# Performance work log

Hardware: AMD Instinct MI355X
Metric: run time of the kernel (lower is better)

Reference implementation:

```python
import jax, jax.numpy as jnp
import numpy as np

B, T, C, H = 128, 256, 384, 6
HS = C // H  # 64
EPS = 1e-5


def _ln(x, g, b):
    mu = jnp.mean(x, axis=-1, keepdims=True)
    var = jnp.mean(jnp.square(x - mu), axis=-1, keepdims=True)
    return (x - mu) * jax.lax.rsqrt(var + EPS) * g + b


def setup_inputs() -> dict:
    key = jax.random.key(0)
    ks = jax.random.split(key, 12)
    s = 0.02
    return {
        "x": jax.random.normal(ks[0], (B, T, C), jnp.float32),
        "wq": jax.random.normal(ks[1], (H, C, HS), jnp.float32) * s,
        "wk": jax.random.normal(ks[2], (H, C, HS), jnp.float32) * s,
        "wv": jax.random.normal(ks[3], (H, C, HS), jnp.float32) * s,
        "w_proj": jax.random.normal(ks[4], (C, C), jnp.float32) * s,
        "b_proj": jax.random.normal(ks[5], (C,), jnp.float32) * s,
        "w1": jax.random.normal(ks[6], (C, 4 * C), jnp.float32) * s,
        "b1": jax.random.normal(ks[7], (4 * C,), jnp.float32) * s,
        "w2": jax.random.normal(ks[8], (4 * C, C), jnp.float32) * s,
        "b2": jax.random.normal(ks[9], (C,), jnp.float32) * s,
        "ln1_g": 1.0 + jax.random.normal(ks[10], (C,), jnp.float32) * s,
        "ln1_b": jnp.zeros((C,), jnp.float32),
        "ln2_g": 1.0 + jax.random.normal(ks[11], (C,), jnp.float32) * s,
        "ln2_b": jnp.zeros((C,), jnp.float32),
    }


def reference(x, wq, wk, wv, w_proj, b_proj, w1, b1, w2, b2, ln1_g, ln1_b, ln2_g, ln2_b):
    # --- attention sublayer (dropout = identity, eval mode) ---
    h = _ln(x, ln1_g, ln1_b)                              # (B,T,C)
    q = jnp.einsum("btc,hcd->bhtd", h, wq)               # (B,H,T,HS)
    k = jnp.einsum("btc,hcd->bhtd", h, wk)
    v = jnp.einsum("btc,hcd->bhtd", h, wv)
    # NOTE: original scales by n_embed**-0.5 (C), not head_size**-0.5
    wei = jnp.einsum("bhtd,bhsd->bhts", q, k) * (C ** -0.5)  # (B,H,T,T)
    tril = jnp.tril(jnp.ones((T, T), bool))
    wei = jnp.where(tril, wei, -jnp.inf)
    # NOTE: original applies softmax over torch dim=1 of (B,T,T) = query axis
    wei = jax.nn.softmax(wei, axis=2)
    attn = jnp.einsum("bhts,bhsd->bhtd", wei, v)          # (B,H,T,HS)
    attn = attn.transpose(0, 2, 1, 3).reshape(B, T, C)    # head-concat order
    x = x + attn @ w_proj + b_proj
    # --- MLP sublayer ---
    h2 = _ln(x, ln2_g, ln2_b)
    x = x + jax.nn.relu(h2 @ w1 + b1) @ w2 + b2
    return x
```

## Files before the change

### kernel.cpp

```cpp
#include <hip/hip_runtime.h>

#define BB 128
#define TT 256
#define CCH 384
#define NHH 6
#define HSZ 64
#define BTT (BB*TT)
#define QKVLD 1152

typedef unsigned short u16;
typedef unsigned int   u32;
typedef __attribute__((ext_vector_type(8))) short  short8;
typedef __attribute__((ext_vector_type(4))) float  floatx4;

__device__ __forceinline__ u16 f2bf(float f) {
  union { float f; u32 i; } v; v.f = f; u32 x = v.i;
  return (u16)((x + 0x7fffu + ((x >> 16) & 1u)) >> 16);
}
__device__ __forceinline__ float bf2f(u16 w) {
  union { u32 i; float f; } v; v.i = ((u32)w) << 16; return v.f;
}

__device__ __forceinline__ void gll16(const u16* g, u16* l) {
  __builtin_amdgcn_global_load_lds((const __attribute__((address_space(1))) void*)g,
                                   (__attribute__((address_space(3))) void*)l, 16, 0, 0);
}

template <int INBF>
__global__ __launch_bounds__(256) void ln_kernel(const void* __restrict__ xv,
                                                 const float* __restrict__ g,
                                                 const float* __restrict__ b,
                                                 u16* __restrict__ out) {
  int row = blockIdx.x * 4 + (threadIdx.x >> 6);
  int lane = threadIdx.x & 63;
  float vals[6];
  float sum = 0.f;
  if (INBF) {
    const u16* xr = (const u16*)xv + (size_t)row * CCH;
#pragma unroll
    for (int i = 0; i < 6; ++i) { vals[i] = bf2f(xr[lane + (i << 6)]); sum += vals[i]; }
  } else {
    const float* xr = (const float*)xv + (size_t)row * CCH;
#pragma unroll
    for (int i = 0; i < 6; ++i) { vals[i] = xr[lane + (i << 6)]; sum += vals[i]; }
  }
#pragma unroll
  for (int off = 32; off; off >>= 1) sum += __shfl_xor(sum, off);
  float mean = sum * (1.f / 384.f);
  float vs = 0.f;
#pragma unroll
  for (int i = 0; i < 6; ++i) { float d = vals[i] - mean; vs += d * d; }
#pragma unroll
  for (int off = 32; off; off >>= 1) vs += __shfl_xor(vs, off);
  float rinv = rsqrtf(vs * (1.f / 384.f) + 1e-5f);
  u16* orow = out + (size_t)row * CCH;
#pragma unroll
  for (int i = 0; i < 6; ++i) {
    int c = lane + (i << 6);
    orow[c] = f2bf((vals[i] - mean) * rinv * g[c] + b[c]);
  }
}

__global__ void repack_all(const float* __restrict__ wq, const float* __restrict__ wk,
                           const float* __restrict__ wv, const float* __restrict__ wproj,
                           const float* __restrict__ w1, const float* __restrict__ w2,
                           u16* __restrict__ wqkv_t, u16* __restrict__ wp_t,
                           u16* __restrict__ w1_t, u16* __restrict__ w2_t) {
  int idx = blockIdx.x * 256 + threadIdx.x;
  if (idx < 147456) {
    int n = idx / CCH, kk = idx % CCH;
    size_t src = ((size_t)(n >> 6) * CCH + kk) * 64 + (n & 63);
    wqkv_t[idx]          = f2bf(wq[src]);
    wqkv_t[idx + 147456] = f2bf(wk[src]);
    wqkv_t[idx + 294912] = f2bf(wv[src]);
  } else if (idx < 294912) {
    int i = idx - 147456;
    int n = i / CCH, kk = i % CCH;
    wp_t[i] = f2bf(wproj[(size_t)kk * CCH + n]);
  } else if (idx < 294912 + 589824) {
    int i = idx - 294912;
    int n = i / CCH, kk = i % CCH;
    w1_t[i] = f2bf(w1[(size_t)kk * 1536 + n]);
  } else if (idx < 294912 + 2 * 589824) {
    int i = idx - 294912 - 589824;
    int n = i / 1536, kk = i % 1536;
    w2_t[i] = f2bf(w2[(size_t)kk * CCH + n]);
  }
}

template <int BIAS, int RES, int RELU, int OUTBF, int RESBF>
__global__ __launch_bounds__(256, 4) void gemm_mfma(const u16* __restrict__ A,
                                                    const u16* __restrict__ W,
                                                    const float* __restrict__ bias,
                                                    const void* __restrict__ resv,
                                                    void* __restrict__ outv,
                                                    int M, int N, int K) {
  __shared__ __align__(16) u16 As[2][128 * 32];
  __shared__ __align__(16) u16 Bs[2][128 * 32];
  const int tid = threadIdx.x;
  const int lane = tid & 63;
  const int w = tid >> 6;
  const int wr = w >> 1, wc = w & 1;

  const int gx = gridDim.x;
  const int nwg = gx * gridDim.y;
  const int bid = blockIdx.y * gx + blockIdx.x;
  const int lin = (bid & 7) * (nwg >> 3) + (bid >> 3);
  const int m0 = (lin / gx) * 128, n0 = (lin % gx) * 128;

  const int lm = lane & 15, qd = lane >> 4;

  floatx4 acc[4][4];
  floatx4 zero4 = {0.f, 0.f, 0.f, 0.f};
#pragma unroll
  for (int i = 0; i < 4; ++i)
#pragma unroll
    for (int j = 0; j < 4; ++j) acc[i][j] = zero4;

  const u16* srcA[2];
  const u16* srcB[2];
#pragma unroll
  for (int c = 0; c < 2; ++c) {
    int row = 32 * w + 16 * c + (lane >> 2);
    int ch = (lane & 3) ^ ((row >> 1) & 3);
    srcA[c] = A + (size_t)(m0 + row) * K + ch * 8;
    srcB[c] = W + (size_t)(n0 + row) * K + ch * 8;
  }
  const int dAB = (32 * w) * 32;

#pragma unroll
  for (int c = 0; c < 2; ++c) gll16(srcA[c], &As[0][dAB + 512 * c]);
#pragma unroll
  for (int c = 0; c < 2; ++c) gll16(srcB[c], &Bs[0][dAB + 512 * c]);

  int ib = 0;
  for (int k0 = 0; k0 < K; k0 += 32, ib ^= 1) {
    __syncthreads();
    int kn = k0 + 32;
    if (kn < K) {
      int nb = ib ^ 1;
#pragma unroll
      for (int c = 0; c < 2; ++c) gll16(srcA[c] + kn, &As[nb][dAB + 512 * c]);
#pragma unroll
      for (int c = 0; c < 2; ++c) gll16(srcB[c] + kn, &Bs[nb][dAB + 512 * c]);
    }
    short8 af[4], bf[4];
#pragma unroll
    for (int i = 0; i < 4; ++i) {
      int rm = 64 * wr + 16 * i + lm;
      af[i] = *(const short8*)&As[ib][rm * 32 + (qd ^ ((rm >> 1) & 3)) * 8];
    }
#pragma unroll
    for (int j = 0; j < 4; ++j) {
      int rn = 64 * wc + 16 * j + lm;
      bf[j] = *(const short8*)&Bs[ib][rn * 32 + (qd ^ ((rn >> 1) & 3)) * 8];
    }
#pragma unroll
    for (int i = 0; i < 4; ++i)
#pragma unroll
      for (int j = 0; j < 4; ++j)
        acc[i][j] = __builtin_amdgcn_mfma_f32_16x16x32_bf16(af[i], bf[j], acc[i][j], 0, 0, 0);
  }

#pragma unroll
  for (int i = 0; i < 4; ++i) {
    int row0 = m0 + 64 * wr + 16 * i + qd * 4;
#pragma unroll
    for (int j = 0; j < 4; ++j) {
      int col = n0 + 64 * wc + 16 * j + lm;
      float bb = 0.f;
      if (BIAS) bb = bias[col];
#pragma unroll
      for (int r = 0; r < 4; ++r) {
        size_t idx = (size_t)(row0 + r) * N + col;
        float val = acc[i][j][r] + bb;
        if (RES) val += RESBF ? bf2f(((const u16*)resv)[idx]) : ((const float*)resv)[idx];
        if (RELU) val = fmaxf(val, 0.f);
        if (OUTBF) ((u16*)outv)[idx] = f2bf(val);
        else       ((float*)outv)[idx] = val;
      }
    }
  }
}

__global__ __launch_bounds__(512, 1) void fused_mlp(const u16* __restrict__ h,
                                                    const u16* __restrict__ w1t,
                                                    const float* __restrict__ b1,
                                                    const u16* __restrict__ w2t,
                                                    const float* __restrict__ b2,
                                                    const u16* __restrict__ x2,
                                                    float* __restrict__ out) {
  __shared__ __align__(16) u16 Ah[128 * 384];
  __shared__ __align__(16) u16 Us[128 * 128];
  const int tid = threadIdx.x;
  const int lane = tid & 63;
  const int w = tid >> 6;
  const int lm = lane & 15, qd = lane >> 4;
  const int m0 = blockIdx.x * 128;

#pragma unroll
  for (int rnd = 0; rnd < 12; ++rnd) {
    int wbase = rnd * 4096 + w * 512;
    int off = wbase + lane * 8;
    int row = off / 384;
    int slot = (off - row * 384) >> 3;
    const u16* src = h + (size_t)(m0 + row) * 384 + ((slot ^ (row & 7)) << 3);
    gll16(src, &Ah[wbase]);
  }
  asm volatile("s_waitcnt vmcnt(0)" ::: "memory");
  __syncthreads();

  floatx4 zero4 = {0.f, 0.f, 0.f, 0.f};
  floatx4 ao[8][3];
#pragma unroll
  for (int i = 0; i < 8; ++i)
#pragma unroll
    for (int j = 0; j < 3; ++j) ao[i][j] = zero4;

  const int wr1 = w >> 2, wc1 = w & 3;

  for (int c = 0; c < 12; ++c) {
    floatx4 au[4][2];
#pragma unroll
    for (int i = 0; i < 4; ++i) { au[i][0] = zero4; au[i][1] = zero4; }
    const u16* w1p = w1t + (size_t)(c * 128 + 32 * wc1 + lm) * 384 + qd * 8;
#pragma unroll
    for (int ks = 0; ks < 12; ++ks) {
      short8 bf0 = *(const short8*)(w1p + ks * 32);
      short8 bf1 = *(const short8*)(w1p + 16 * 384 + ks * 32);
      int sl = ((ks * 4 + qd) ^ (lm & 7)) << 3;
#pragma unroll
      for (int i = 0; i < 4; ++i) {
        short8 af = *(const short8*)&Ah[(64 * wr1 + 16 * i + lm) * 384 + sl];
        au[i][0] = __builtin_amdgcn_mfma_f32_16x16x32_bf16(af, bf0, au[i][0], 0, 0, 0);
        au[i][1] = __builtin_amdgcn_mfma_f32_16x16x32_bf16(af, bf1, au[i][1], 0, 0, 0);
      }
    }
    float bv0 = b1[c * 128 + 32 * wc1 + lm];
    float bv1 = b1[c * 128 + 32 * wc1 + 16 + lm];
#pragma unroll
    for (int i = 0; i < 4; ++i)
#pragma unroll
      for (int j = 0; j < 2; ++j) {
        int ucol = 32 * wc1 + 16 * j + lm;
        float bv = j ? bv1 : bv0;
#pragma unroll
        for (int r = 0; r < 4; ++r) {
          int urow = 64 * wr1 + 16 * i + qd * 4 + r;
          float v = fmaxf(au[i][j][r] + bv, 0.f);
          Us[urow * 128 + ((((ucol >> 3) ^ (urow & 7)) << 3) | (ucol & 7))] = f2bf(v);
        }
      }
    __syncthreads();

    const u16* w2p = w2t + (size_t)(48 * w + lm) * 1536 + c * 128 + qd * 8;
#pragma unroll
    for (int ks = 0; ks < 4; ++ks) {
      short8 bb0 = *(const short8*)(w2p + ks * 32);
      short8 bb1 = *(const short8*)(w2p + (size_t)16 * 1536 + ks * 32);
      short8 bb2 = *(const short8*)(w2p + (size_t)32 * 1536 + ks * 32);
      int sl = ((ks * 4 + qd) ^ (lm & 7)) << 3;
#pragma unroll
      for (int i = 0; i < 8; ++i) {
        short8 uf = *(const short8*)&Us[(16 * i + lm) * 128 + sl];
        ao[i][0] = __builtin_amdgcn_mfma_f32_16x16x32_bf16(uf, bb0, ao[i][0], 0, 0, 0);
        ao[i][1] = __builtin_amdgcn_mfma_f32_16x16x32_bf16(uf, bb1, ao[i][1], 0, 0, 0);
        ao[i][2] = __builtin_amdgcn_mfma_f32_16x16x32_bf16(uf, bb2, ao[i][2], 0, 0, 0);
      }
    }
    __syncthreads();
  }

#pragma unroll
  for (int i = 0; i < 8; ++i)
#pragma unroll
    for (int jj = 0; jj < 3; ++jj) {
      int col = 48 * w + 16 * jj + lm;
      float bb = b2[col];
#pragma unroll
      for (int r = 0; r < 4; ++r) {
        size_t idx = (size_t)(m0 + 16 * i + qd * 4 + r) * 384 + col;
        out[idx] = ao[i][jj][r] + bb + bf2f(x2[idx]);
      }
    }
}

#define ASCALE 0.051031036307982884f

__global__ __launch_bounds__(1024) void attn_mfma(const u16* __restrict__ qkv,
                                                  u16* __restrict__ out) {
  __shared__ __align__(16) char lds_raw[36864 + 20480 + 2048];
  u16*   Ks       = (u16*)lds_raw;
  u16*   VT       = (u16*)lds_raw;
  float* partials = (float*)(lds_raw + 36864);
  u16*   stage    = (u16*)(lds_raw + 36864);
  float* gmax     = (float*)(lds_raw + 57344);
  float* linv     = (float*)(lds_raw + 58368);

  const int tid = threadIdx.x;
  const int lane = tid & 63;
  const int w = tid >> 6;
  const int lm = lane & 15, qd = lane >> 4;
  const int b = blockIdx.x / NHH, h = blockIdx.x % NHH;
  const size_t rowbase = (size_t)b * TT;
  const u16* qp = qkv + rowbase * QKVLD + h * HSZ;
  const u16* kp = qp + 384;
  const u16* vp = qp + 768;

  {
    int s = tid >> 2, c4 = tid & 3;
    const u16* src = kp + (size_t)s * QKVLD;
    *(uint4*)&Ks[s * 72 + c4 * 8]       = *(const uint4*)(src + c4 * 8);
    *(uint4*)&Ks[s * 72 + (c4 + 4) * 8] = *(const uint4*)(src + (c4 + 4) * 8);
  }
  short8 qf0, qf1;
  {
    const u16* qrow = qp + (size_t)(16 * w + lm) * QKVLD + qd * 8;
    qf0 = *(const short8*)(qrow);
    qf1 = *(const short8*)(qrow + 32);
  }
  __syncthreads();

  floatx4 acc[16];
  floatx4 zero4 = {0.f, 0.f, 0.f, 0.f};
#pragma unroll
  for (int tc = 0; tc < 16; ++tc) acc[tc] = zero4;

#pragma unroll
  for (int tc = 0; tc < 16; ++tc) {
    if (tc <= w) {
      int sr = 16 * tc + lm;
      short8 kf0 = *(const short8*)&Ks[sr * 72 + qd * 8];
      short8 kf1 = *(const short8*)&Ks[sr * 72 + 32 + qd * 8];
      acc[tc] = __builtin_amdgcn_mfma_f32_16x16x32_bf16(qf0, kf0, acc[tc], 0, 0, 0);
      acc[tc] = __builtin_amdgcn_mfma_f32_16x16x32_bf16(qf1, kf1, acc[tc], 0, 0, 0);
    }
  }

  const int rb = 16 * w + qd * 4;
  float pmax[16];
#pragma unroll
  for (int tc = 0; tc < 16; ++tc) {
    float m = -1e30f;
    if (tc <= w) {
      int sc = 16 * tc + lm;
#pragma unroll
      for (int r = 0; r < 4; ++r) {
        float vv = acc[tc][r] * ASCALE;
        vv = (rb + r >= sc) ? vv : -1e30f;
        acc[tc][r] = vv;
        m = fmaxf(m, vv);
      }
    }
    m = fmaxf(m, __shfl_xor(m, 16));
    m = fmaxf(m, __shfl_xor(m, 32));
    pmax[tc] = m;
  }
  if (lane < 16) {
#pragma unroll
    for (int tc = 0; tc < 16; ++tc) partials[w * 256 + tc * 16 + lane] = pmax[tc];
  }
  __syncthreads();
  if (tid < 256) {
    float m = partials[tid];
#pragma unroll
    for (int i = 1; i < 16; ++i) m = fmaxf(m, partials[i * 256 + tid]);
    gmax[tid] = m;
  }
  __syncthreads();

  float psum[16];
#pragma unroll
  for (int tc = 0; tc < 16; ++tc) {
    float s = 0.f;
    if (tc <= w) {
      float gm = gmax[tc * 16 + lm];
#pragma unroll
      for (int r = 0; r < 4; ++r) {
        float e = (acc[tc][r] > -1e29f) ? __expf(acc[tc][r] - gm) : 0.f;
        acc[tc][r] = e;
        s += e;
      }
    }
    s += __shfl_xor(s, 16);
    s += __shfl_xor(s, 32);
    psum[tc] = s;
  }
  if (lane < 16) {
#pragma unroll
    for (int tc = 0; tc < 16; ++tc) partials[w * 256 + tc * 16 + lane] = psum[tc];
  }
  __syncthreads();
  if (tid < 256) {
    float s = partials[tid];
#pragma unroll
    for (int i = 1; i < 16; ++i) s += partials[i * 256 + tid];
    linv[tid] = 1.f / s;
  }
  __syncthreads();

  {
    int s = tid >> 2, dg = (tid & 3) * 16;
    const u16* vrow = vp + (size_t)s * QKVLD + dg;
    u16 tmp[16];
    *(uint4*)&tmp[0] = *(const uint4*)(vrow);
    *(uint4*)&tmp[8] = *(const uint4*)(vrow + 8);
#pragma unroll
    for (int j = 0; j < 16; ++j) VT[(dg + j) * 264 + s] = tmp[j];
  }
  __syncthreads();

  u16* mst = stage + w * 640;
  floatx4 oacc[4];
#pragma unroll
  for (int nt = 0; nt < 4; ++nt) oacc[nt] = zero4;

#pragma unroll
  for (int c = 0; c < 8; ++c) {
    if (2 * c <= w) {
#pragma unroll
      for (int tt = 0; tt < 2; ++tt) {
        int tc = 2 * c + tt;
        float li = (tc <= w) ? linv[tc * 16 + lm] : 0.f;
#pragma unroll
        for (int r = 0; r < 4; ++r) {
          float pv = (tc <= w) ? acc[tc][r] * li : 0.f;
          mst[(qd * 4 + r) * 40 + tt * 16 + lm] = f2bf(pv);
        }
      }
      asm volatile("s_waitcnt lgkmcnt(0)" ::: "memory");
      short8 pf = *(const short8*)&mst[lm * 40 + qd * 8];
#pragma unroll
      for (int nt = 0; nt < 4; ++nt) {
        short8 vf = *(const short8*)&VT[(nt * 16 + lm) * 264 + c * 32 + qd * 8];
        oacc[nt] = __builtin_amdgcn_mfma_f32_16x16x32_bf16(pf, vf, oacc[nt], 0, 0, 0);
      }
      asm volatile("" ::: "memory");
    }
  }

  u16* ob = out + rowbase * CCH + h * HSZ;
#pragma unroll
  for (int nt = 0; nt < 4; ++nt) {
#pragma unroll
    for (int r = 0; r < 4; ++r) {
      int t = 16 * w + qd * 4 + r;
      ob[(size_t)t * CCH + nt * 16 + lm] = f2bf(oacc[nt][r]);
    }
  }
}

extern "C" void kernel_launch(void* const* d_in, const int* in_sizes, int n_in,
                              void* d_out, int out_size, void* d_ws, size_t ws_size,
                              hipStream_t stream) {
  const float* x     = (const float*)d_in[0];
  const float* wq    = (const float*)d_in[1];
  const float* wk    = (const float*)d_in[2];
  const float* wv    = (const float*)d_in[3];
  const float* wproj = (const float*)d_in[4];
  const float* bproj = (const float*)d_in[5];
  const float* w1    = (const float*)d_in[6];
  const float* b1    = (const float*)d_in[7];
  const float* w2    = (const float*)d_in[8];
  const float* b2    = (const float*)d_in[9];
  const float* ln1g  = (const float*)d_in[10];
  const float* ln1b  = (const float*)d_in[11];
  const float* ln2g  = (const float*)d_in[12];
  const float* ln2b  = (const float*)d_in[13];
  float* out = (float*)d_out;
  (void)in_sizes; (void)n_in; (void)out_size; (void)ws_size;

  char* ws = (char*)d_ws;
  size_t off = 0;
  auto alloc = [&](size_t bytes) -> void* {
    void* p = ws + off;
    off += (bytes + 255) & ~(size_t)255;
    return p;
  };

  u16* wqkv_t = (u16*)alloc((size_t)QKVLD * CCH * 2);
  u16* wp_t   = (u16*)alloc((size_t)CCH * CCH * 2);
  u16* w1_t   = (u16*)alloc((size_t)4 * CCH * CCH * 2);
  u16* w2_t   = (u16*)alloc((size_t)CCH * 4 * CCH * 2);
  u16*   h_b  = (u16*)alloc((size_t)BTT * CCH * 2);
  u16*   x2   = (u16*)alloc((size_t)BTT * CCH * 2);
  u16*   qkv_b = (u16*)alloc((size_t)BTT * 4 * CCH * 2);

  repack_all<<<5760, 256, 0, stream>>>(wq, wk, wv, wproj, w1, w2,
                                       wqkv_t, wp_t, w1_t, w2_t);

  ln_kernel<0><<<BTT / 4, 256, 0, stream>>>(x, ln1g, ln1b, h_b);

  gemm_mfma<0, 0, 0, 1, 0><<<dim3(9, 256), 256, 0, stream>>>(h_b, wqkv_t, nullptr, nullptr,
                                                             qkv_b, BTT, QKVLD, CCH);
  attn_mfma<<<BB * NHH, 1024, 0, stream>>>(qkv_b, h_b);

  gemm_mfma<1, 1, 0, 1, 0><<<dim3(3, 256), 256, 0, stream>>>(h_b, wp_t, bproj, x, x2,
                                                             BTT, CCH, CCH);
  ln_kernel<1><<<BTT / 4, 256, 0, stream>>>(x2, ln2g, ln2b, h_b);

  fused_mlp<<<256, 512, 0, stream>>>(h_b, w1_t, b1, w2_t, b2, x2, out);
}
```

Before: 388.8 us.

## Halve fused MLP row tile, compute transposed hidden tile, raise occupancy

The fused MLP kernel now processes 64 rows per block instead of 128 and launches 512 blocks, with launch bounds requesting up to 4 blocks per CU. It also swaps MFMA operands so each wave computes a transposed 16x64 hidden slice, which lets the bias load as a vector and the ReLU output be packed into 4-element LDS stores with a new XOR swizzle. The goal is more resident waves and better CU fill, in exchange for each block reusing every W1/W2 fragment over fewer rows, which roughly doubles weight traffic from L2.

```diff
diff --git a/kernel.cpp b/kernel.cpp
--- a/kernel.cpp
+++ b/kernel.cpp
@@ -11,6 +11,7 @@
 typedef unsigned short u16;
 typedef unsigned int   u32;
 typedef __attribute__((ext_vector_type(8))) short  short8;
+typedef __attribute__((ext_vector_type(4))) short  short4v;
 typedef __attribute__((ext_vector_type(4))) float  floatx4;
 
 __device__ __forceinline__ u16 f2bf(float f) {
@@ -183,23 +184,23 @@
   }
 }
 
-__global__ __launch_bounds__(512, 1) void fused_mlp(const u16* __restrict__ h,
+__global__ __launch_bounds__(512, 4) void fused_mlp(const u16* __restrict__ h,
                                                     const u16* __restrict__ w1t,
                                                     const float* __restrict__ b1,
                                                     const u16* __restrict__ w2t,
                                                     const float* __restrict__ b2,
                                                     const u16* __restrict__ x2,
                                                     float* __restrict__ out) {
-  __shared__ __align__(16) u16 Ah[128 * 384];
-  __shared__ __align__(16) u16 Us[128 * 128];
+  __shared__ __align__(16) u16 Ah[64 * 384];
+  __shared__ __align__(16) u16 Us[64 * 128];
   const int tid = threadIdx.x;
   const int lane = tid & 63;
   const int w = tid >> 6;
   const int lm = lane & 15, qd = lane >> 4;
-  const int m0 = blockIdx.x * 128;
-
-#pragma unroll
-  for (int rnd = 0; rnd < 12; ++rnd) {
+  const int m0 = blockIdx.x * 64;
+
+#pragma unroll
+  for (int rnd = 0; rnd < 6; ++rnd) {
     int wbase = rnd * 4096 + w * 512;
     int off = wbase + lane * 8;
     int row = off / 384;
@@ -211,68 +212,67 @@
   __syncthreads();
 
   floatx4 zero4 = {0.f, 0.f, 0.f, 0.f};
-  floatx4 ao[8][3];
-#pragma unroll
-  for (int i = 0; i < 8; ++i)
+  floatx4 ao[4][3];
+#pragma unroll
+  for (int i = 0; i < 4; ++i)
 #pragma unroll
     for (int j = 0; j < 3; ++j) ao[i][j] = zero4;
 
-  const int wr1 = w >> 2, wc1 = w & 3;
-
   for (int c = 0; c < 12; ++c) {
-    floatx4 au[4][2];
-#pragma unroll
-    for (int i = 0; i < 4; ++i) { au[i][0] = zero4; au[i][1] = zero4; }
-    const u16* w1p = w1t + (size_t)(c * 128 + 32 * wc1 + lm) * 384 + qd * 8;
+    floatx4 au[4];
+#pragma unroll
+    for (int mt = 0; mt < 4; ++mt) au[mt] = zero4;
+    const u16* w1p = w1t + (size_t)(c * 128 + 16 * w + lm) * 384 + qd * 8;
 #pragma unroll
     for (int ks = 0; ks < 12; ++ks) {
-      short8 bf0 = *(const short8*)(w1p + ks * 32);
-      short8 bf1 = *(const short8*)(w1p + 16 * 384 + ks * 32);
+      short8 wf = *(const short8*)(w1p + ks * 32);
       int sl = ((ks * 4 + qd) ^ (lm & 7)) << 3;
 #pragma unroll
+      for (int mt = 0; mt < 4; ++mt) {
+        short8 hf = *(const short8*)&Ah[(16 * mt + lm) * 384 + sl];
+        au[mt] = __builtin_amdgcn_mfma_f32_16x16x32_bf16(wf, hf, au[mt], 0, 0, 0);
+      }
+    }
+    floatx4 bv = *(const floatx4*)&b1[c * 128 + 16 * w + qd * 4];
+    short4v upk[4];
+#pragma unroll
+    for (int mt = 0; mt < 4; ++mt)
+#pragma unroll
+      for (int r = 0; r < 4; ++r)
+        upk[mt][r] = (short)f2bf(fmaxf(au[mt][r] + bv[r], 0.f));
+
+    __syncthreads();
+    {
+      int s8 = ((4 * w + qd) ^ lm) * 4;
+#pragma unroll
+      for (int mt = 0; mt < 4; ++mt)
+        *(short4v*)&Us[(16 * mt + lm) * 128 + s8] = upk[mt];
+    }
+    __syncthreads();
+
+    const u16* w2p = w2t + (size_t)(48 * w + lm) * 1536 + c * 128 + qd * 8;
+#pragma unroll
+    for (int ks = 0; ks < 4; ++ks) {
+      short8 wb0 = *(const short8*)(w2p + ks * 32);
+      short8 wb1 = *(const short8*)(w2p + (size_t)16 * 1536 + ks * 32);
+      short8 wb2 = *(const short8*)(w2p + (size_t)32 * 1536 + ks * 32);
+      int sa = (((ks * 8 + qd * 2) ^ lm)) * 4;
+      int sb = (((ks * 8 + qd * 2 + 1) ^ lm)) * 4;
+#pragma unroll
       for (int i = 0; i < 4; ++i) {
-        short8 af = *(const short8*)&Ah[(64 * wr1 + 16 * i + lm) * 384 + sl];
-        au[i][0] = __builtin_amdgcn_mfma_f32_16x16x32_bf16(af, bf0, au[i][0], 0, 0, 0);
-        au[i][1] = __builtin_amdgcn_mfma_f32_16x16x32_bf16(af, bf1, au[i][1], 0, 0, 0);
-      }
-    }
-    float bv0 = b1[c * 128 + 32 * wc1 + lm];
-    float bv1 = b1[c * 128 + 32 * wc1 + 16 + lm];
-#pragma unroll
-    for (int i = 0; i < 4; ++i)
-#pragma unroll
-      for (int j = 0; j < 2; ++j) {
-        int ucol = 32 * wc1 + 16 * j + lm;
-        float bv = j ? bv1 : bv0;
-#pragma unroll
-        for (int r = 0; r < 4; ++r) {
-          int urow = 64 * wr1 + 16 * i + qd * 4 + r;
-          float v = fmaxf(au[i][j][r] + bv, 0.f);
-          Us[urow * 128 + ((((ucol >> 3) ^ (urow & 7)) << 3) | (ucol & 7))] = f2bf(v);
-        }
-      }
-    __syncthreads();
-
-    const u16* w2p = w2t + (size_t)(48 * w + lm) * 1536 + c * 128 + qd * 8;
-#pragma unroll
-    for (int ks = 0; ks < 4; ++ks) {
-      short8 bb0 = *(const short8*)(w2p + ks * 32);
-      short8 bb1 = *(const short8*)(w2p + (size_t)16 * 1536 + ks * 32);
-      short8 bb2 = *(const short8*)(w2p + (size_t)32 * 1536 + ks * 32);
-      int sl = ((ks * 4 + qd) ^ (lm & 7)) << 3;
-#pragma unroll
-      for (int i = 0; i < 8; ++i) {
-        short8 uf = *(const short8*)&Us[(16 * i + lm) * 128 + sl];
-        ao[i][0] = __builtin_amdgcn_mfma_f32_16x16x32_bf16(uf, bb0, ao[i][0], 0, 0, 0);
-        ao[i][1] = __builtin_amdgcn_mfma_f32_16x16x32_bf16(uf, bb1, ao[i][1], 0, 0, 0);
-        ao[i][2] = __builtin_amdgcn_mfma_f32_16x16x32_bf16(uf, bb2, ao[i][2], 0, 0, 0);
-      }
-    }
-    __syncthreads();
-  }
-
-#pragma unroll
-  for (int i = 0; i < 8; ++i)
+        int rb = (16 * i + lm) * 128;
+        short4v u0 = *(const short4v*)&Us[rb + sa];
+        short4v u1 = *(const short4v*)&Us[rb + sb];
+        short8 uf = {u0[0], u0[1], u0[2], u0[3], u1[0], u1[1], u1[2], u1[3]};
+        ao[i][0] = __builtin_amdgcn_mfma_f32_16x16x32_bf16(uf, wb0, ao[i][0], 0, 0, 0);
+        ao[i][1] = __builtin_amdgcn_mfma_f32_16x16x32_bf16(uf, wb1, ao[i][1], 0, 0, 0);
+        ao[i][2] = __builtin_amdgcn_mfma_f32_16x16x32_bf16(uf, wb2, ao[i][2], 0, 0, 0);
+      }
+    }
+  }
+
+#pragma unroll
+  for (int i = 0; i < 4; ++i)
 #pragma unroll
     for (int jj = 0; jj < 3; ++jj) {
       int col = 48 * w + 16 * jj + lm;
@@ -499,5 +499,5 @@
                                                              BTT, CCH, CCH);
   ln_kernel<1><<<BTT / 4, 256, 0, stream>>>(x2, ln2g, ln2b, h_b);
 
-  fused_mlp<<<256, 512, 0, stream>>>(h_b, w1_t, b1, w2_t, b2, x2, out);
-}
+  fused_mlp<<<512, 512, 0, stream>>>(h_b, w1_t, b1, w2_t, b2, x2, out);
+}
```

Result: slower. 397.5 us (+2.2%).
